# Performance work log

Hardware: AMD Instinct MI355X
Metric: run time of the kernel (lower is better)

## Reference

```python
import jax, jax.numpy as jnp
import numpy as np

N_GRAPHS = 500
NODES_PER_GRAPH = 200
EDGES_PER_GRAPH = 6400
N = N_GRAPHS * NODES_PER_GRAPH          # 100000 nodes
E = N_GRAPHS * EDGES_PER_GRAPH          # 3200000 edges
D = 256                                  # dim_hidden
RATIO = 0.8
EPS = 1e-12


def setup_inputs() -> dict:
    key = jax.random.key(0)
    k1, k2 = jax.random.split(key, 2)
    x = jax.random.normal(k1, (N, D), dtype=jnp.float32)
    # edges consistent with batch: both endpoints inside the same graph
    rng = np.random.default_rng(0)
    g = np.repeat(np.arange(N_GRAPHS, dtype=np.int32), EDGES_PER_GRAPH)
    row = g * NODES_PER_GRAPH + rng.integers(0, NODES_PER_GRAPH, E).astype(np.int32)
    col = g * NODES_PER_GRAPH + rng.integers(0, NODES_PER_GRAPH, E).astype(np.int32)
    edge_index = jnp.asarray(np.stack([row, col]), dtype=jnp.int32)
    batch = jnp.asarray(np.repeat(np.arange(N_GRAPHS, dtype=np.int32), NODES_PER_GRAPH))
    W = jax.random.normal(k2, (2 * D, 1), dtype=jnp.float32) * (1.0 / np.sqrt(2 * D))
    b = jnp.zeros((1,), dtype=jnp.float32)
    return {"x": x, "edge_index": edge_index, "batch": batch, "W": W, "b": b}


def _edge_scores(x, W, b, edge_index):
    # concat(x[row], x[col]) @ W == (x @ W_row)[row] + (x @ W_col)[col]
    # -> avoids materializing the [E, 2D] edge_rep tensor.
    row, col = edge_index[0], edge_index[1]
    s_row = x @ W[:D, 0]   # [N]
    s_col = x @ W[D:, 0]   # [N]
    return s_row[row] + s_col[col] + b[0]  # [E]


def _topk_edge_mask(edge_score, edge_graph):
    # sparse_sort (descending=True): norm = minmax(score) - graph_id; argsort desc.
    f_min, f_max = edge_score.min(), edge_score.max()
    norm = (edge_score - f_min) / (f_max - f_min + EPS) - edge_graph.astype(edge_score.dtype)
    perm = jnp.argsort(-norm)  # graphs ascending, score descending within graph
    deg = jax.ops.segment_sum(jnp.ones_like(edge_graph), edge_graph, num_segments=N_GRAPHS)
    k = jnp.ceil(RATIO * deg.astype(jnp.float32)).astype(deg.dtype)
    start = jnp.concatenate([jnp.zeros((1,), deg.dtype), jnp.cumsum(deg)[:-1]])
    sg = edge_graph[perm]                        # graph id in sorted order
    pos = jnp.arange(E, dtype=deg.dtype) - start[sg]  # rank within segment
    keep_sorted = pos < k[sg]
    # scatter keep flags back to original edge order
    return jnp.zeros((E,), dtype=bool).at[perm].set(keep_sorted)


def _relabel(x, batch, edge_index, emask):
    # padded equivalent of torch.unique + scatter relabel:
    # selected nodes are compacted to the front of x/batch; dropped slots -> -1.
    row, col = edge_index[0], edge_index[1]
    m = emask.astype(jnp.int32)
    sel = (jnp.zeros((N,), jnp.int32).at[row].max(m).at[col].max(m)).astype(bool)
    new_id = jnp.where(sel, jnp.cumsum(sel) - 1, -1)           # [N]
    new_ei = jnp.where(emask[None, :], new_id[edge_index], -1)  # [2, E], -1 = padding
    order = jnp.argsort(~sel)                                   # stable: selected first
    x_out = x[order]                                            # [N, D], selected at front
    batch_out = jnp.where(sel[order], batch[order], -1)
    return x_out, new_ei, batch_out, sel.sum()


def reference(x, edge_index, batch, W, b):
    edge_score = _edge_scores(x, W, b, edge_index)
    edge_graph = batch[edge_index[0]]
    mask = _topk_edge_mask(edge_score, edge_graph)   # True = causal edge
    causal_w = jnp.where(mask, edge_score, 0.0)
    conf_w = jnp.where(mask, 0.0, -edge_score)
    causal_x, causal_ei, causal_batch, n_causal = _relabel(x, batch, edge_index, mask)
    conf_x, conf_ei, conf_batch, n_conf = _relabel(x, batch, edge_index, ~mask)
    return (causal_x, causal_ei, causal_w, causal_batch, n_causal,
            conf_x, conf_ei, conf_w, conf_batch, n_conf,
            edge_score, mask)
```

## Files before the change

kernel.cpp:

```cpp
#include <hip/hip_runtime.h>
#include <cmath>

typedef unsigned long long u64;
typedef unsigned int u32;
typedef unsigned char u8;

#define DHID 256
#define NMAX 100000
#define EMAX 3200000
#define EPGMAX 6400
#define NBLKMAX 128
#define TOPK_T 512

__device__ float g_srow[NMAX];
__device__ float g_scol[NMAX];
__device__ float g_escore[EMAX];
__device__ int   g_destC[NMAX];
__device__ int   g_destF[NMAX];
__device__ u8    g_selC[NMAX];
__device__ u8    g_selF[NMAX];
__device__ u8    g_mask[EMAX];
__device__ float g_pmin[1024];
__device__ float g_pmax[1024];
__device__ float g_fmm[2];
__device__ int   g_blkC[NBLKMAX];
__device__ int   g_blkF[NBLKMAX];
__device__ int   g_tot[2];

__global__ void k_node_scores(const float* __restrict__ x, const float* __restrict__ W, int N){
  int t = blockIdx.x*256 + threadIdx.x;
  if (t < N){ g_selC[t] = 0; g_selF[t] = 0; }
  int lane = threadIdx.x & 63, wave = threadIdx.x >> 6;
  int n = blockIdx.x*4 + wave;
  if (n >= N) return;
  float4 xv = ((const float4*)(x + (size_t)n*DHID))[lane];
  float4 wr = ((const float4*)W)[lane];
  float4 wc = ((const float4*)W)[64 + lane];
  double dr = (double)xv.x*wr.x + (double)xv.y*wr.y + (double)xv.z*wr.z + (double)xv.w*wr.w;
  double dc = (double)xv.x*wc.x + (double)xv.y*wc.y + (double)xv.z*wc.z + (double)xv.w*wc.w;
  #pragma unroll
  for (int off = 32; off; off >>= 1){
    dr += __shfl_xor(dr, off);
    dc += __shfl_xor(dc, off);
  }
  if (lane == 0){ g_srow[n] = (float)dr; g_scol[n] = (float)dc; }
}

__global__ void k_minmax_part(const int* __restrict__ ei, const float* __restrict__ b, int E){
  float b0 = b[0];
  float lmin = INFINITY, lmax = -INFINITY;
  for (int e = blockIdx.x*256 + threadIdx.x; e < E; e += gridDim.x*256){
    int r = ei[e], c = ei[E + e];
    float s = (g_srow[r] + g_scol[c]) + b0;
    g_escore[e] = s;
    lmin = fminf(lmin, s); lmax = fmaxf(lmax, s);
  }
  __shared__ float smin[256], smax[256];
  smin[threadIdx.x] = lmin; smax[threadIdx.x] = lmax;
  __syncthreads();
  for (int st = 128; st; st >>= 1){
    if (threadIdx.x < st){
      smin[threadIdx.x] = fminf(smin[threadIdx.x], smin[threadIdx.x+st]);
      smax[threadIdx.x] = fmaxf(smax[threadIdx.x], smax[threadIdx.x+st]);
    }
    __syncthreads();
  }
  if (threadIdx.x == 0){ g_pmin[blockIdx.x] = smin[0]; g_pmax[blockIdx.x] = smax[0]; }
}

__global__ void k_minmax_final(int nb){
  float lmin = INFINITY, lmax = -INFINITY;
  for (int i = threadIdx.x; i < nb; i += 256){
    lmin = fminf(lmin, g_pmin[i]); lmax = fmaxf(lmax, g_pmax[i]);
  }
  __shared__ float smin[256], smax[256];
  smin[threadIdx.x] = lmin; smax[threadIdx.x] = lmax;
  __syncthreads();
  for (int st = 128; st; st >>= 1){
    if (threadIdx.x < st){
      smin[threadIdx.x] = fminf(smin[threadIdx.x], smin[threadIdx.x+st]);
      smax[threadIdx.x] = fmaxf(smax[threadIdx.x], smax[threadIdx.x+st]);
    }
    __syncthreads();
  }
  if (threadIdx.x == 0){ g_fmm[0] = smin[0]; g_fmm[1] = smax[0]; }
}

__global__ __launch_bounds__(TOPK_T) void k_topk(const int* __restrict__ ei,
    int E, int EPG, int k){
  __shared__ u32 keys[EPGMAX];
  __shared__ int hist[256];
  __shared__ int scan[256];
  __shared__ int tscan[TOPK_T];
  __shared__ u32 sh_prefix;
  __shared__ int sh_rem, sh_rem_next, sh_digit;
  int g = blockIdx.x, tid = threadIdx.x;
  long long base = (long long)g * EPG;
  float fmin = g_fmm[0], fmax = g_fmm[1];
  float denom = (fmax - fmin) + 1e-12f;
  float gf = (float)g;

  for (int i = tid; i < EPG; i += TOPK_T){
    float s = g_escore[base + i];
    float frac = (s - fmin) / denom;
    float nk = frac - gf;
    u32 u = __float_as_uint(nk);
    u = (u & 0x80000000u) ? ~u : (u | 0x80000000u);
    keys[i] = ~u;
  }
  if (tid == 0){ sh_prefix = 0; sh_rem = k; }
  __syncthreads();

  for (int shift = 24; shift >= 0; shift -= 8){
    if (tid < 256) hist[tid] = 0;
    __syncthreads();
    u32 pref = sh_prefix;
    int lane = tid & 63;
    for (int i = tid; i < EPG; i += TOPK_T){
      u32 kk = keys[i];
      bool cand = (shift == 24) || ((kk >> (shift + 8)) == pref);
      if (cand){
        u32 digit = (kk >> shift) & 0xFF;
        u32 d0 = __builtin_amdgcn_readfirstlane(digit);
        if (__all(digit == d0)){
          u64 m = __ballot(1);
          if (lane == __builtin_ctzll(m)) atomicAdd(&hist[d0], (int)__popcll(m));
        } else {
          atomicAdd(&hist[digit], 1);
        }
      }
    }
    __syncthreads();
    if (tid < 256) scan[tid] = hist[tid];
    __syncthreads();
    for (int st = 1; st < 256; st <<= 1){
      int t2 = (tid < 256 && tid >= st) ? scan[tid - st] : 0;
      __syncthreads();
      if (tid < 256) scan[tid] += t2;
      __syncthreads();
    }
    if (tid < 256){
      int rem = sh_rem;
      int cumprev = tid ? scan[tid - 1] : 0;
      if (cumprev < rem && rem <= scan[tid]){
        sh_digit = tid;
        sh_rem_next = rem - cumprev;
      }
    }
    __syncthreads();
    if (tid == 0){
      sh_prefix = (sh_prefix << 8) | (u32)sh_digit;
      sh_rem = sh_rem_next;
    }
    __syncthreads();
  }
  u32 T = sh_prefix;
  int r_budget = sh_rem;

  int CH = (EPG + TOPK_T - 1) / TOPK_T;
  int c0 = tid * CH;
  int cnt = 0;
  for (int j = 0; j < CH; j++){
    int i = c0 + j;
    if (i < EPG && keys[i] == T) cnt++;
  }
  tscan[tid] = cnt;
  __syncthreads();
  for (int st = 1; st < TOPK_T; st <<= 1){
    int t2 = (tid >= st) ? tscan[tid - st] : 0;
    __syncthreads();
    tscan[tid] += t2;
    __syncthreads();
  }
  int rank = tid ? tscan[tid - 1] : 0;

  for (int j = 0; j < CH; j++){
    int i = c0 + j;
    if (i >= EPG) break;
    u32 kk = keys[i];
    int kept;
    if (kk < T) kept = 1;
    else if (kk == T){ kept = (rank < r_budget); rank++; }
    else kept = 0;
    long long e = base + i;
    int rr = ei[e], cc = ei[E + e];
    g_mask[e] = (u8)kept;
    if (kept){ g_selC[rr] = 1; g_selC[cc] = 1; }
    else     { g_selF[rr] = 1; g_selF[cc] = 1; }
  }
}

__global__ void k_blocksum(int N){
  int bb = blockIdx.x, tid = threadIdx.x;
  int start = bb*1024;
  int c = 0, f = 0;
  #pragma unroll
  for (int q = 0; q < 4; q++){
    int n = start + tid*4 + q;
    if (n < N){ c += g_selC[n]; f += g_selF[n]; }
  }
  __shared__ int sc[256], sf[256];
  sc[tid] = c; sf[tid] = f;
  __syncthreads();
  for (int st = 128; st; st >>= 1){
    if (tid < st){ sc[tid] += sc[tid+st]; sf[tid] += sf[tid+st]; }
    __syncthreads();
  }
  if (tid == 0){ g_blkC[bb] = sc[0]; g_blkF[bb] = sf[0]; }
}

__global__ void k_scanblk(int nb, float* __restrict__ out, long long oNC, long long oNF){
  if (blockIdx.x == 0 && threadIdx.x == 0){
    int accC = 0, accF = 0;
    for (int i = 0; i < nb; i++){
      int c = g_blkC[i], f = g_blkF[i];
      g_blkC[i] = accC; g_blkF[i] = accF;
      accC += c; accF += f;
    }
    g_tot[0] = accC; g_tot[1] = accF;
    out[oNC] = (float)accC;
    out[oNF] = (float)accF;
  }
}

__global__ void k_dest(const int* __restrict__ batch,
    float* __restrict__ out, long long oCB, long long oFB, int N){
  int bb = blockIdx.x, tid = threadIdx.x;
  int start = bb*1024;
  int idx0 = start + tid*4;
  int c[4], f[4]; int sc = 0, sf = 0;
  #pragma unroll
  for (int q = 0; q < 4; q++){
    int n = idx0 + q;
    int vc = (n < N) ? (int)g_selC[n] : 0;
    int vf = (n < N) ? (int)g_selF[n] : 0;
    c[q] = vc; f[q] = vf; sc += vc; sf += vf;
  }
  __shared__ int xc[256], xf[256];
  xc[tid] = sc; xf[tid] = sf;
  __syncthreads();
  for (int st = 1; st < 256; st <<= 1){
    int ac = (tid >= st) ? xc[tid-st] : 0;
    int af = (tid >= st) ? xf[tid-st] : 0;
    __syncthreads();
    xc[tid] += ac; xf[tid] += af;
    __syncthreads();
  }
  int excC = ((tid ? xc[tid-1] : 0)) + g_blkC[bb];
  int excF = ((tid ? xf[tid-1] : 0)) + g_blkF[bb];
  int nC = g_tot[0], nF = g_tot[1];
  int runC = 0, runF = 0;
  #pragma unroll
  for (int q = 0; q < 4; q++){
    int n = idx0 + q;
    if (n >= N) break;
    runC += c[q]; runF += f[q];
    int cumC = excC + runC;
    int cumF = excF + runF;
    int dC = c[q] ? (cumC - 1) : (nC + (n - cumC));
    int dF = f[q] ? (cumF - 1) : (nF + (n - cumF));
    dC = min(max(dC, 0), N-1);
    dF = min(max(dF, 0), N-1);
    g_destC[n] = dC; g_destF[n] = dF;
    float bt = (float)batch[n];
    out[oCB + dC] = c[q] ? bt : -1.0f;
    out[oFB + dF] = f[q] ? bt : -1.0f;
  }
}

__global__ void k_edges_out(const int* __restrict__ ei, const float* __restrict__ b,
    float* __restrict__ out, long long oCE, long long oCW, long long oFE, long long oFW,
    long long oS, long long oM, int E){
  int e = blockIdx.x*256 + threadIdx.x;
  if (e >= E) return;
  int r = ei[e], c = ei[E + e];
  float s = (g_srow[r] + g_scol[c]) + b[0];
  int m = g_mask[e];
  out[oCE + e]     = m ? (float)g_destC[r] : -1.0f;
  out[oCE + E + e] = m ? (float)g_destC[c] : -1.0f;
  out[oCW + e]     = m ? s : 0.0f;
  out[oFE + e]     = m ? -1.0f : (float)g_destF[r];
  out[oFE + E + e] = m ? -1.0f : (float)g_destF[c];
  out[oFW + e]     = m ? 0.0f : -s;
  out[oS + e]      = s;
  out[oM + e]      = m ? 1.0f : 0.0f;
}

__global__ void k_x_out(const float* __restrict__ x, float* __restrict__ out,
    long long oCX, long long oFX, int N){
  long long t = (long long)blockIdx.x*256 + threadIdx.x;
  if (t >= (long long)N*64) return;
  int n = (int)(t >> 6), cq = (int)(t & 63);
  float4 v = ((const float4*)x)[(long long)n*64 + cq];
  int dC = g_destC[n], dF = g_destF[n];
  long long iC = oCX + (long long)dC*DHID + cq*4;
  *reinterpret_cast<float4*>(out + iC) = v;
  long long iF = oFX + (long long)dF*DHID + cq*4;
  out[iF+0] = v.x; out[iF+1] = v.y; out[iF+2] = v.z; out[iF+3] = v.w;
}

extern "C" void kernel_launch(void* const* d_in, const int* in_sizes, int n_in,
                              void* d_out, int out_size, void* d_ws, size_t ws_size,
                              hipStream_t stream) {
  const float* x   = (const float*)d_in[0];
  const int* ei    = (const int*)d_in[1];
  const int* batch = (const int*)d_in[2];
  const float* W   = (const float*)d_in[3];
  const float* b   = (const float*)d_in[4];
  float* out = (float*)d_out;

  int N   = in_sizes[0] / DHID;
  int E   = in_sizes[1] / 2;
  if (N > NMAX) N = NMAX;
  if (E > EMAX) E = EMAX;
  const int G   = N / 200;
  int EPG = (G > 0) ? E / G : 0;
  if (EPG > EPGMAX) EPG = EPGMAX;
  const int k   = (int)ceilf(0.8f * (float)EPG);

  long long oCX = 0;
  long long oCE = oCX + (long long)N*DHID;
  long long oCW = oCE + 2LL*E;
  long long oCB = oCW + E;
  long long oNC = oCB + N;
  long long oFX = oNC + 1;
  long long oFE = oFX + (long long)N*DHID;
  long long oFW = oFE + 2LL*E;
  long long oFB = oFW + E;
  long long oNF = oFB + N;
  long long oS  = oNF + 1;
  long long oM  = oS + E;

  k_node_scores<<<(N + 3)/4, 256, 0, stream>>>(x, W, N);
  k_minmax_part<<<1024, 256, 0, stream>>>(ei, b, E);
  k_minmax_final<<<1, 256, 0, stream>>>(1024);
  k_topk<<<G, TOPK_T, 0, stream>>>(ei, E, EPG, k);
  int nblk = (N + 1023)/1024;
  k_blocksum<<<nblk, 256, 0, stream>>>(N);
  k_scanblk<<<1, 64, 0, stream>>>(nblk, out, oNC, oNF);
  k_dest<<<nblk, 256, 0, stream>>>(batch, out, oCB, oFB, N);
  k_edges_out<<<(E + 255)/256, 256, 0, stream>>>(ei, b, out, oCE, oCW, oFE, oFW, oS, oM, E);
  k_x_out<<<(int)(((long long)N*64 + 255)/256), 256, 0, stream>>>(x, out, oCX, oFX, N);
}
```

Before: 195.1 us.

## Fuse min/max finalize and edge score outputs into topk, parallelize block scan

Removes the single-block min/max finalize kernel by having every topk block reduce the 1024 partials itself. The topk kernel now stages keep flags in shared memory and writes mask, score and weight outputs with coalesced strided stores, so the edge output kernel no longer regathers node scores. The serial block-offset scan becomes a shared-memory parallel scan, and the unaligned conf-x store uses a float2 for its middle elements. The cost is a redundant reduction in each of the 500 blocks and extra shared memory in topk.

```diff
diff --git a/kernel.cpp b/kernel.cpp
--- a/kernel.cpp
+++ b/kernel.cpp
@@ -22,7 +22,6 @@
 __device__ u8    g_mask[EMAX];
 __device__ float g_pmin[1024];
 __device__ float g_pmax[1024];
-__device__ float g_fmm[2];
 __device__ int   g_blkC[NBLKMAX];
 __device__ int   g_blkF[NBLKMAX];
 __device__ int   g_tot[2];
@@ -68,35 +67,39 @@
   if (threadIdx.x == 0){ g_pmin[blockIdx.x] = smin[0]; g_pmax[blockIdx.x] = smax[0]; }
 }
 
-__global__ void k_minmax_final(int nb){
-  float lmin = INFINITY, lmax = -INFINITY;
-  for (int i = threadIdx.x; i < nb; i += 256){
-    lmin = fminf(lmin, g_pmin[i]); lmax = fmaxf(lmax, g_pmax[i]);
-  }
-  __shared__ float smin[256], smax[256];
-  smin[threadIdx.x] = lmin; smax[threadIdx.x] = lmax;
-  __syncthreads();
-  for (int st = 128; st; st >>= 1){
-    if (threadIdx.x < st){
-      smin[threadIdx.x] = fminf(smin[threadIdx.x], smin[threadIdx.x+st]);
-      smax[threadIdx.x] = fmaxf(smax[threadIdx.x], smax[threadIdx.x+st]);
-    }
-    __syncthreads();
-  }
-  if (threadIdx.x == 0){ g_fmm[0] = smin[0]; g_fmm[1] = smax[0]; }
-}
-
 __global__ __launch_bounds__(TOPK_T) void k_topk(const int* __restrict__ ei,
+    float* __restrict__ out, long long oCW, long long oFW, long long oS, long long oM,
     int E, int EPG, int k){
   __shared__ u32 keys[EPGMAX];
+  __shared__ u8  keep[EPGMAX];
   __shared__ int hist[256];
   __shared__ int scan[256];
   __shared__ int tscan[TOPK_T];
+  __shared__ float redA[TOPK_T];
   __shared__ u32 sh_prefix;
   __shared__ int sh_rem, sh_rem_next, sh_digit;
   int g = blockIdx.x, tid = threadIdx.x;
   long long base = (long long)g * EPG;
-  float fmin = g_fmm[0], fmax = g_fmm[1];
+
+  float lmin = fminf(g_pmin[tid], g_pmin[tid + 512]);
+  float lmax = fmaxf(g_pmax[tid], g_pmax[tid + 512]);
+  redA[tid] = lmin;
+  __syncthreads();
+  for (int st = 256; st; st >>= 1){
+    if (tid < st) redA[tid] = fminf(redA[tid], redA[tid+st]);
+    __syncthreads();
+  }
+  float fmin = redA[0];
+  __syncthreads();
+  redA[tid] = lmax;
+  __syncthreads();
+  for (int st = 256; st; st >>= 1){
+    if (tid < st) redA[tid] = fmaxf(redA[tid], redA[tid+st]);
+    __syncthreads();
+  }
+  float fmax = redA[0];
+  __syncthreads();
+
   float denom = (fmax - fmin) + 1e-12f;
   float gf = (float)g;
 
@@ -182,9 +185,20 @@
     if (kk < T) kept = 1;
     else if (kk == T){ kept = (rank < r_budget); rank++; }
     else kept = 0;
+    keep[i] = (u8)kept;
+  }
+  __syncthreads();
+
+  for (int i = tid; i < EPG; i += TOPK_T){
     long long e = base + i;
+    int kept = keep[i];
+    float s = g_escore[e];
     int rr = ei[e], cc = ei[E + e];
     g_mask[e] = (u8)kept;
+    out[oS + e]  = s;
+    out[oM + e]  = kept ? 1.0f : 0.0f;
+    out[oCW + e] = kept ? s : 0.0f;
+    out[oFW + e] = kept ? 0.0f : -s;
     if (kept){ g_selC[rr] = 1; g_selC[cc] = 1; }
     else     { g_selF[rr] = 1; g_selF[cc] = 1; }
   }
@@ -210,16 +224,24 @@
 }
 
 __global__ void k_scanblk(int nb, float* __restrict__ out, long long oNC, long long oNF){
-  if (blockIdx.x == 0 && threadIdx.x == 0){
-    int accC = 0, accF = 0;
-    for (int i = 0; i < nb; i++){
-      int c = g_blkC[i], f = g_blkF[i];
-      g_blkC[i] = accC; g_blkF[i] = accF;
-      accC += c; accF += f;
-    }
-    g_tot[0] = accC; g_tot[1] = accF;
-    out[oNC] = (float)accC;
-    out[oNF] = (float)accF;
+  __shared__ int sC[NBLKMAX], sF[NBLKMAX];
+  int tid = threadIdx.x;
+  int c = (tid < nb) ? g_blkC[tid] : 0;
+  int f = (tid < nb) ? g_blkF[tid] : 0;
+  sC[tid] = c; sF[tid] = f;
+  __syncthreads();
+  for (int st = 1; st < NBLKMAX; st <<= 1){
+    int a  = (tid >= st) ? sC[tid - st] : 0;
+    int b2 = (tid >= st) ? sF[tid - st] : 0;
+    __syncthreads();
+    sC[tid] += a; sF[tid] += b2;
+    __syncthreads();
+  }
+  if (tid < nb){ g_blkC[tid] = sC[tid] - c; g_blkF[tid] = sF[tid] - f; }
+  if (tid == NBLKMAX - 1){
+    g_tot[0] = sC[NBLKMAX-1]; g_tot[1] = sF[NBLKMAX-1];
+    out[oNC] = (float)sC[NBLKMAX-1];
+    out[oNF] = (float)sF[NBLKMAX-1];
   }
 }
 
@@ -268,22 +290,16 @@
   }
 }
 
-__global__ void k_edges_out(const int* __restrict__ ei, const float* __restrict__ b,
-    float* __restrict__ out, long long oCE, long long oCW, long long oFE, long long oFW,
-    long long oS, long long oM, int E){
+__global__ void k_ei_out(const int* __restrict__ ei,
+    float* __restrict__ out, long long oCE, long long oFE, int E){
   int e = blockIdx.x*256 + threadIdx.x;
   if (e >= E) return;
   int r = ei[e], c = ei[E + e];
-  float s = (g_srow[r] + g_scol[c]) + b[0];
   int m = g_mask[e];
   out[oCE + e]     = m ? (float)g_destC[r] : -1.0f;
   out[oCE + E + e] = m ? (float)g_destC[c] : -1.0f;
-  out[oCW + e]     = m ? s : 0.0f;
   out[oFE + e]     = m ? -1.0f : (float)g_destF[r];
   out[oFE + E + e] = m ? -1.0f : (float)g_destF[c];
-  out[oFW + e]     = m ? 0.0f : -s;
-  out[oS + e]      = s;
-  out[oM + e]      = m ? 1.0f : 0.0f;
 }
 
 __global__ void k_x_out(const float* __restrict__ x, float* __restrict__ out,
@@ -296,7 +312,10 @@
   long long iC = oCX + (long long)dC*DHID + cq*4;
   *reinterpret_cast<float4*>(out + iC) = v;
   long long iF = oFX + (long long)dF*DHID + cq*4;
-  out[iF+0] = v.x; out[iF+1] = v.y; out[iF+2] = v.z; out[iF+3] = v.w;
+  out[iF] = v.x;
+  float2 mid; mid.x = v.y; mid.y = v.z;
+  *reinterpret_cast<float2*>(out + iF + 1) = mid;
+  out[iF + 3] = v.w;
 }
 
 extern "C" void kernel_launch(void* const* d_in, const int* in_sizes, int n_in,
@@ -333,12 +352,11 @@
 
   k_node_scores<<<(N + 3)/4, 256, 0, stream>>>(x, W, N);
   k_minmax_part<<<1024, 256, 0, stream>>>(ei, b, E);
-  k_minmax_final<<<1, 256, 0, stream>>>(1024);
-  k_topk<<<G, TOPK_T, 0, stream>>>(ei, E, EPG, k);
+  k_topk<<<G, TOPK_T, 0, stream>>>(ei, out, oCW, oFW, oS, oM, E, EPG, k);
   int nblk = (N + 1023)/1024;
   k_blocksum<<<nblk, 256, 0, stream>>>(N);
-  k_scanblk<<<1, 64, 0, stream>>>(nblk, out, oNC, oNF);
+  k_scanblk<<<1, NBLKMAX, 0, stream>>>(nblk, out, oNC, oNF);
   k_dest<<<nblk, 256, 0, stream>>>(batch, out, oCB, oFB, N);
-  k_edges_out<<<(E + 255)/256, 256, 0, stream>>>(ei, b, out, oCE, oCW, oFE, oFW, oS, oM, E);
+  k_ei_out<<<(E + 255)/256, 256, 0, stream>>>(ei, out, oCE, oFE, E);
   k_x_out<<<(int)(((long long)N*64 + 255)/256), 256, 0, stream>>>(x, out, oCX, oFX, N);
 }
```

New measurement: 171.3 us. 1.14x faster.
